# Kernel tuning notes

Hardware: AMD Instinct MI355X
Metric: run time of the kernel (lower is better)

Reference implementation:

```python
import jax, jax.numpy as jnp
import numpy as np

NB, H, C = 6, 4, 192
B, S, L = 2, 64, 256
VOCAB, ED = 24, 64


def setup_inputs() -> dict:
    key = jax.random.key(0)
    ks = iter(jax.random.split(key, 32))
    r = lambda sh: jax.random.normal(next(ks), sh, jnp.float32) * 0.02
    z = lambda sh: jnp.zeros(sh, jnp.float32)
    return {
        'tokens': jax.random.randint(next(ks), (B, S, L), 0, VOCAB, jnp.int32),
        'emb': r((VOCAB, ED)),
        'proj_w': r((C, ED)), 'proj_b': z((C,)),
        'ln_g': jnp.ones((NB, 3, C), jnp.float32), 'ln_b': z((NB, 3, C)),
        'wq': r((NB, 2, C, C)), 'wk': r((NB, 2, C, C)),
        'wv': r((NB, 2, C, C)), 'wo': r((NB, 2, C, C)),
        'bq': z((NB, 2, C)), 'bk': z((NB, 2, C)),
        'bv': z((NB, 2, C)), 'bo': z((NB, 2, C)),
        'ffn_w1': r((NB, 4 * C, C)), 'ffn_b1': z((NB, 4 * C)),
        'ffn_w2': r((NB, C, 4 * C)), 'ffn_b2': z((NB, C)),
        'pw_w': r((C,)), 'pw_b': z(()),
    }


def rotary(x):
    # ESM-style rotary embedding over positions along dim -2, feature dim last.
    d = x.shape[-1]
    inv = 1.0 / (10000.0 ** (jnp.arange(0, d, 2, dtype=jnp.float32) / d))
    t = jnp.arange(x.shape[-2], dtype=jnp.float32)
    f = t[:, None] * inv[None, :]                  # (pos, d/2)
    emb = jnp.concatenate([f, f], axis=-1)         # (pos, d)
    cos, sin = jnp.cos(emb), jnp.sin(emb)
    x1, x2 = jnp.split(x, 2, axis=-1)
    return x * cos + jnp.concatenate([-x2, x1], axis=-1) * sin


def ln_ch(x, g, b, eps=1e-5):
    # LayerNorm over channel axis 1 of (B,C,X,Y) (== transpose->LN->transpose).
    m = x.mean(axis=1, keepdims=True)
    v = jnp.var(x, axis=1, keepdims=True)
    return (x - m) * jax.lax.rsqrt(v + eps) * g[None, :, None, None] + b[None, :, None, None]


def lin_attn(x, wq, wk, wv, wo, bq, bk, bv, bo):
    # ScaledLinearAttention: elu+1 feature map, attends over dim -2 of (B,A,N,C).
    Bm, A, N, Cm = x.shape
    dh = Cm // H
    sh = lambda t: t.reshape(Bm, A, N, H, dh).transpose(0, 1, 3, 2, 4)  # (B,A,H,N,dh)
    q = sh(x @ wq.T + bq)
    k = sh(x @ wk.T + bk)
    v = sh(x @ wv.T + bv)
    q = (jax.nn.elu(q) + 1.0) / jnp.sqrt(jnp.float32(dh))
    k = jax.nn.elu(k) + 1.0
    kv = jnp.einsum('bahnd,bahne->bahde', k, v)
    z = 1.0 / (jnp.einsum('bahnd,bahd->bahn', q, k.sum(axis=-2)) + 1e-6)
    o = jnp.einsum('bahnd,bahde->bahne', q, kv) * z[..., None]
    o = o.transpose(0, 1, 3, 2, 4).reshape(Bm, A, N, Cm)
    return o @ wo.T + bo


def fwd(tokens, emb, proj_w, proj_b, ln_g, ln_b, wq, wk, wv, wo, bq, bk, bv, bo,
        ffn_w1, ffn_b1, ffn_w2, ffn_b2, pw_w, pw_b):
    x = emb[tokens]                    # (B,S,L,ED)
    x = x @ proj_w.T + proj_b          # (B,S,L,C)
    x = rotary(x)                      # rotary over L positions
    out = jnp.transpose(x, (0, 3, 1, 2))  # (B,C,S,L)
    for i in range(NB):
        # row attention (over L)
        h = ln_ch(out, ln_g[i, 0], ln_b[i, 0])
        h = jnp.transpose(h, (0, 2, 3, 1))  # (B,S,L,C)
        h = lin_attn(h, wq[i, 0], wk[i, 0], wv[i, 0], wo[i, 0],
                     bq[i, 0], bk[i, 0], bv[i, 0], bo[i, 0])
        out = out + jnp.transpose(h, (0, 3, 1, 2))
        # col attention (over S)
        h = ln_ch(out, ln_g[i, 1], ln_b[i, 1])
        h = jnp.transpose(h, (0, 3, 2, 1))  # (B,L,S,C)
        h = lin_attn(h, wq[i, 1], wk[i, 1], wv[i, 1], wo[i, 1],
                     bq[i, 1], bk[i, 1], bv[i, 1], bo[i, 1])
        out = out + jnp.transpose(h, (0, 3, 2, 1))
        # 1x1-conv FFN
        h = ln_ch(out, ln_g[i, 2], ln_b[i, 2])
        h = jnp.einsum('bcxy,oc->boxy', h, ffn_w1[i]) + ffn_b1[i][None, :, None, None]
        h = jax.nn.gelu(h, approximate=False)
        h = jnp.einsum('bcxy,oc->boxy', h, ffn_w2[i]) + ffn_b2[i][None, :, None, None]
        out = out + h
    o = jnp.einsum('bcxy,c->bxy', out, pw_w) + pw_b   # pwFNN 1x1 conv to 1 ch
    return jax.nn.sigmoid(jax.nn.softplus(o))


def reference(tokens, emb, proj_w, proj_b, ln_g, ln_b, wq, wk, wv, wo, bq, bk, bv, bo,
              ffn_w1, ffn_b1, ffn_w2, ffn_b2, pw_w, pw_b):
    return fwd(tokens, emb, proj_w, proj_b, ln_g, ln_b, wq, wk, wv, wo, bq, bk, bv, bo,
               ffn_w1, ffn_b1, ffn_w2, ffn_b2, pw_w, pw_b)
```

## Files before the change

kernel.cpp:

```cpp
#include <hip/hip_runtime.h>
#include <hip/hip_bf16.h>
#include <math.h>

#define NBLK 6
#define NH 4
#define CCH 192
#define BB 2
#define SS 64
#define LL 256
#define DH 48
#define NP (BB*SS*LL)
#define BUF ((size_t)NP*CCH)

typedef __attribute__((ext_vector_type(8))) short short8;
typedef __attribute__((ext_vector_type(4))) float float4v;
typedef __attribute__((ext_vector_type(2))) unsigned int uintx2;

__device__ __forceinline__ unsigned short f2b(float f) {
    union { float f; unsigned int u; } v; v.f = f;
    unsigned int r = v.u + 0x7FFF + ((v.u >> 16) & 1);
    return (unsigned short)(r >> 16);
}
__device__ __forceinline__ float b2f(unsigned short u) {
    union { unsigned int u; float f; } v; v.u = ((unsigned int)u) << 16;
    return v.f;
}
__device__ __forceinline__ unsigned int cvt_pk_bf16(float lo, float hi) {
    unsigned int r;
    asm("v_cvt_pk_bf16_f32 %0, %1, %2" : "=v"(r) : "v"(lo), "v"(hi));
    return r;
}
__device__ __forceinline__ void st2u(unsigned short* p0, unsigned short* p1, float a, float b) {
    unsigned int u = cvt_pk_bf16(a, b);
    *p0 = (unsigned short)u;
    *p1 = (unsigned short)(u >> 16);
}
__device__ __forceinline__ void xf_unpack(uintx2 u, float* f) {
    union { unsigned int x; float ff; } t;
    t.x = u[0] << 16;          f[0] = t.ff;
    t.x = u[0] & 0xffff0000u;  f[1] = t.ff;
    t.x = u[1] << 16;          f[2] = t.ff;
    t.x = u[1] & 0xffff0000u;  f[3] = t.ff;
}
__device__ __forceinline__ float gelu_f(float v) {
    float z = v * 0.7071067811865475f;
    float a = fabsf(z);
    float t = __builtin_amdgcn_rcpf(fmaf(0.3275911f, a, 1.0f));
    float p = fmaf(t, 1.061405429f, -1.453152027f);
    p = fmaf(t, p, 1.421413741f);
    p = fmaf(t, p, -0.284496736f);
    p = fmaf(t, p, 0.254829592f);
    p *= t;
    float e = __expf(-a * a);
    float er = fmaf(-p, e, 1.0f);
    er = __builtin_copysignf(er, z);
    return 0.5f * v * (1.0f + er);
}
__device__ __forceinline__ void async_lds16(const void* g, void* l) {
    __builtin_amdgcn_global_load_lds(
        (const __attribute__((address_space(1))) unsigned int*)g,
        (__attribute__((address_space(3))) unsigned int*)l, 16, 0, 0);
}

#define XF(p16, c) (((size_t)(p16) * 192 + (c)) << 4)

template<int N, int K>
__global__ void swz_conv(const float* __restrict__ src, unsigned short* __restrict__ dst, int layers) {
    int s = blockIdx.x * 256 + threadIdx.x;
    if (s >= layers * N * K) return;
    int li = s / (N * K);
    int t = s - li * (N * K);
    constexpr int KC = K / 32;
    int chunk = t >> 9, c = t & 511;
    int g = chunk / KC, sk = chunk - g * KC;
    int lane = c >> 3, ko = c & 7;
    int n = g * 16 + (lane & 15), k = sk * 32 + (lane >> 4) * 8 + ko;
    dst[s] = f2b(src[(size_t)li * N * K + (size_t)n * K + k]);
}
__global__ void wqkv_swz(const float* __restrict__ wq, const float* __restrict__ wk,
                         const float* __restrict__ wv, unsigned short* __restrict__ d) {
    int s = blockIdx.x * 256 + threadIdx.x;
    int wi = s / (576 * 192);
    int t = s - wi * 576 * 192;
    int chunk = t >> 9, c = t & 511;
    int g = chunk / 6, sk = chunk - g * 6;
    int lane = c >> 3, ko = c & 7;
    int n = g * 16 + (lane & 15), k = sk * 32 + (lane >> 4) * 8 + ko;
    int sg = n / 192, row = n - sg * 192;
    const float* src = (sg == 0) ? wq : (sg == 1) ? wk : wv;
    d[s] = f2b(src[(size_t)wi * 192 * 192 + (size_t)row * 192 + k]);
}
__global__ void bqkv_concat(const float* __restrict__ bq, const float* __restrict__ bk,
                            const float* __restrict__ bv, float* __restrict__ d) {
    int idx = blockIdx.x * 256 + threadIdx.x;
    if (idx >= NBLK * 2 * 576) return;
    int wi = idx / 576, n = idx - (idx / 576) * 576;
    int sg = n / 192, row = n - sg * 192;
    const float* src = (sg == 0) ? bq : (sg == 1) ? bk : bv;
    d[idx] = src[wi * CCH + row];
}

__global__ void gather_kernel(const int* __restrict__ tokens, const float* __restrict__ emb,
                              unsigned short* __restrict__ Eg) {
    int idx = blockIdx.x * 256 + threadIdx.x;
    int p = idx >> 6, c = idx & 63;
    Eg[idx] = f2b(emb[tokens[p] * 64 + c]);
}

__global__ __launch_bounds__(256) void rotary_ln_kernel(const float* __restrict__ Xt,
                                                        unsigned short* __restrict__ X,
                                                        unsigned short* __restrict__ Hn,
                                                        const float* __restrict__ g, const float* __restrict__ b) {
    int wave = threadIdx.x >> 6;
    int lane = threadIdx.x & 63;
    int p = blockIdx.x * 4 + wave;
    int l = p & (LL - 1);
    const float* xp = Xt + (size_t)p * CCH;
    float v[3];
    #pragma unroll
    for (int i = 0; i < 3; ++i) {
        int c = lane + i * 64;
        int j = c % 96;
        float inv = expf((float)(2 * j) * (-9.210340371976184f / 192.0f));
        float ang = (float)l * inv;
        float part = (c < 96) ? -xp[c + 96] : xp[c - 96];
        v[i] = xp[c] * cosf(ang) + part * sinf(ang);
    }
    float s = v[0] + v[1] + v[2];
    float qq = v[0] * v[0] + v[1] * v[1] + v[2] * v[2];
    #pragma unroll
    for (int off = 32; off; off >>= 1) {
        s += __shfl_xor(s, off, 64);
        qq += __shfl_xor(qq, off, 64);
    }
    float mean = s * (1.0f / 192.0f);
    float var = qq * (1.0f / 192.0f) - mean * mean;
    float r = rsqrtf(var + 1e-5f);
    unsigned short* hp = Hn + (size_t)p * CCH;
    const int p16 = p >> 4, pr = p & 15;
    #pragma unroll
    for (int i = 0; i < 3; ++i) {
        int c = lane + i * 64;
        X[XF(p16, c) + pr] = f2b(v[i]);
        hp[c] = f2b((v[i] - mean) * r * g[c] + b[c]);
    }
}

template<int MT, int EPI>
__global__ __launch_bounds__(256, (MT == 128) ? 3 : 4)
void mm192(const unsigned short* __restrict__ A, const unsigned short* __restrict__ Wsw,
           const float* __restrict__ bias,
           unsigned short* __restrict__ O0, unsigned short* __restrict__ O1,
           unsigned short* __restrict__ O2,
           float* __restrict__ Of,
           int M, int N, int K) {
    constexpr int NI = MT / 32;
    __shared__ __align__(16) unsigned char lds[(MT == 128) ? 51200 : 28672];
    const int tid = threadIdx.x;
    const int lane = tid & 63;
    const int w = tid >> 6;
    const int wm = w >> 1, wn = w & 1;
    const int m0 = blockIdx.y * MT;
    const int g0 = blockIdx.x * 12;
    const int q = lane >> 4;
    const int q8 = q << 3;
    const int r15 = lane & 15;
    const int KC = K >> 5;

    for (int c = w; c < (MT / 16) * KC; c += 4) {
        int g = c / KC, sk = c - g * KC;
        async_lds16(A + (size_t)(m0 + g * 16 + r15) * K + sk * 32 + q8, lds + c * 1024);
    }

    float4v acc[NI][6];
    #pragma unroll
    for (int i = 0; i < NI; ++i)
        #pragma unroll
        for (int j = 0; j < 6; ++j)
            acc[i][j] = (float4v){0.f, 0.f, 0.f, 0.f};

    __syncthreads();

    for (int sk = 0; sk < KC; ++sk) {
        short8 af[NI], wf[6];
        #pragma unroll
        for (int j = 0; j < 6; ++j)
            wf[j] = *(const short8*)(Wsw + (((size_t)(g0 + wn * 6 + j) * KC + sk) << 9) + lane * 8);
        #pragma unroll
        for (int i = 0; i < NI; ++i)
            af[i] = *(const short8*)(lds + (((wm * NI + i) * KC + sk) << 10) + lane * 16);
        #pragma unroll
        for (int i = 0; i < NI; ++i)
            #pragma unroll
            for (int j = 0; j < 6; ++j)
                acc[i][j] = __builtin_amdgcn_mfma_f32_16x16x32_bf16(af[i], wf[j], acc[i][j], 0, 0, 0);
    }

    const int nb = blockIdx.x * 192 + wn * 96 + r15;
    const int mb = m0 + wm * (MT / 2) + q * 4;

    if (EPI == 0) {
        const int bx = blockIdx.x;
        unsigned short* dst = (bx == 0) ? O0 : (bx == 1) ? O1 : O2;
        #pragma unroll
        for (int j = 0; j < 6; ++j) {
            int n = nb + j * 16;
            int col = wn * 96 + j * 16 + r15;
            float bv = bias[n];
            #pragma unroll
            for (int i = 0; i < NI; ++i) {
                int mrow = wm * (MT / 2) + i * 16 + q * 4;
                #pragma unroll
                for (int r = 0; r < 4; ++r) {
                    float v = acc[i][j][r] + bv;
                    if (bx < 2) v = (v > 0.f) ? v + 1.f : __expf(v);
                    if (bx == 0) v *= 0.14433756729740643f;
                    dst[(size_t)(m0 + mrow + r) * 192 + col] = f2b(v);
                }
            }
        }
    } else {
        #pragma unroll
        for (int j = 0; j < 6; ++j) {
            int n = nb + j * 16;
            float bv = bias[n];
            #pragma unroll
            for (int i = 0; i < NI; ++i) {
                int mrow = mb + i * 16;
                #pragma unroll
                for (int r = 0; r < 4; ++r)
                    Of[(size_t)(mrow + r) * N + n] = acc[i][j][r] + bv;
            }
        }
    }
}


__global__ __launch_bounds__(256, 2)
void wo_qkv(const unsigned short* __restrict__ Ho,
            const unsigned short* __restrict__ WOs, const float* __restrict__ BO,
            unsigned short* __restrict__ Xres,
            const float* __restrict__ lng, const float* __restrict__ lnb,
            const unsigned short* __restrict__ QKVs, const float* __restrict__ bqkv,
            unsigned short* __restrict__ Qb, unsigned short* __restrict__ Kb,
            unsigned short* __restrict__ Vb) {
    __shared__ __align__(16) unsigned char lds[51200];
    unsigned char* Lo = lds;
    float* lsum = (float*)(lds + 24576);
    float* lsq  = lsum + 256;
    unsigned char* Ap = lds + 26624;
    const int tid = threadIdx.x;
    const int lane = tid & 63;
    const int w = tid >> 6;
    const int m0 = blockIdx.x * 64;
    const int q = lane >> 4, q8 = q << 3, r15 = lane & 15;
    const int nb = w * 48 + r15;

    #pragma unroll
    for (int it = 0; it < 6; ++it) {
        int c = it * 4 + w;
        int g = c / 6, sk = c - g * 6;
        async_lds16(Ho + (size_t)(m0 + g * 16 + r15) * 192 + sk * 32 + q8, Lo + c * 1024);
    }
    __syncthreads();

    float4v acc[4][3];
    #pragma unroll
    for (int i = 0; i < 4; ++i)
        #pragma unroll
        for (int j = 0; j < 3; ++j)
            acc[i][j] = (float4v){0.f, 0.f, 0.f, 0.f};
    #pragma unroll
    for (int kk = 0; kk < 6; ++kk) {
        short8 af[4], wf[3];
        #pragma unroll
        for (int j = 0; j < 3; ++j)
            wf[j] = *(const short8*)(WOs + (((size_t)(w * 3 + j) * 6 + kk) << 9) + lane * 8);
        #pragma unroll
        for (int i = 0; i < 4; ++i)
            af[i] = *(const short8*)(Lo + ((i * 6 + kk) << 10) + lane * 16);
        #pragma unroll
        for (int i = 0; i < 4; ++i)
            #pragma unroll
            for (int j = 0; j < 3; ++j)
                acc[i][j] = __builtin_amdgcn_mfma_f32_16x16x32_bf16(af[i], wf[j], acc[i][j], 0, 0, 0);
    }

    #pragma unroll
    for (int j = 0; j < 3; ++j) {
        int n = nb + j * 16;
        float bv = BO[n];
        #pragma unroll
        for (int i = 0; i < 4; ++i) {
            unsigned short* xp = Xres + XF(blockIdx.x * 4 + i, n) + q * 4;
            uintx2 u = *(const uintx2*)xp;
            float f[4]; xf_unpack(u, f);
            #pragma unroll
            for (int r = 0; r < 4; ++r) acc[i][j][r] += bv + f[r];
            uintx2 o;
            o[0] = cvt_pk_bf16(acc[i][j][0], acc[i][j][1]);
            o[1] = cvt_pk_bf16(acc[i][j][2], acc[i][j][3]);
            *(uintx2*)xp = o;
        }
    }
    #pragma unroll
    for (int i = 0; i < 4; ++i)
        #pragma unroll
        for (int r = 0; r < 4; ++r) {
            float s1 = acc[i][0][r] + acc[i][1][r] + acc[i][2][r];
            float s2 = acc[i][0][r] * acc[i][0][r] + acc[i][1][r] * acc[i][1][r] + acc[i][2][r] * acc[i][2][r];
            #pragma unroll
            for (int off = 1; off < 16; off <<= 1) {
                s1 += __shfl_xor(s1, off, 64);
                s2 += __shfl_xor(s2, off, 64);
            }
            if (r15 == 0) {
                int rl = i * 16 + q * 4 + r;
                lsum[rl * 4 + w] = s1;
                lsq[rl * 4 + w] = s2;
            }
        }
    __syncthreads();
    #pragma unroll
    for (int i = 0; i < 4; ++i) {
        float mean[4], rstd[4];
        #pragma unroll
        for (int r = 0; r < 4; ++r) {
            int rl4 = (i * 16 + q * 4 + r) * 4;
            float s  = lsum[rl4] + lsum[rl4 + 1] + lsum[rl4 + 2] + lsum[rl4 + 3];
            float ss = lsq[rl4] + lsq[rl4 + 1] + lsq[rl4 + 2] + lsq[rl4 + 3];
            float m = s * (1.0f / 192.0f);
            mean[r] = m;
            rstd[r] = rsqrtf(ss * (1.0f / 192.0f) - m * m + 1e-5f);
        }
        #pragma unroll
        for (int j = 0; j < 3; ++j) {
            int h = nb + j * 16;
            float gg = lng[h], bb = lnb[h];
            unsigned short* ap = (unsigned short*)Ap + (i * 6 + (h >> 5)) * 512
                               + ((h >> 3) & 3) * 128 + (h & 7) + q * 32;
            float v0 = (acc[i][j][0] - mean[0]) * rstd[0] * gg + bb;
            float v1 = (acc[i][j][1] - mean[1]) * rstd[1] * gg + bb;
            float v2 = (acc[i][j][2] - mean[2]) * rstd[2] * gg + bb;
            float v3 = (acc[i][j][3] - mean[3]) * rstd[3] * gg + bb;
            st2u(ap, ap + 8, v0, v1);
            st2u(ap + 16, ap + 24, v2, v3);
        }
    }
    __syncthreads();

    for (int seg = 0; seg < 3; ++seg) {
        float4v a2[4][3];
        #pragma unroll
        for (int i = 0; i < 4; ++i)
            #pragma unroll
            for (int j = 0; j < 3; ++j)
                a2[i][j] = (float4v){0.f, 0.f, 0.f, 0.f};
        #pragma unroll
        for (int kk = 0; kk < 6; ++kk) {
            short8 af[4], wf[3];
            #pragma unroll
            for (int j = 0; j < 3; ++j)
                wf[j] = *(const short8*)(QKVs + (((size_t)(seg * 12 + w * 3 + j) * 6 + kk) << 9) + lane * 8);
            #pragma unroll
            for (int i = 0; i < 4; ++i)
                af[i] = *(const short8*)(Ap + ((i * 6 + kk) << 10) + lane * 16);
            #pragma unroll
            for (int i = 0; i < 4; ++i)
                #pragma unroll
                for (int j = 0; j < 3; ++j)
                    a2[i][j] = __builtin_amdgcn_mfma_f32_16x16x32_bf16(af[i], wf[j], a2[i][j], 0, 0, 0);
        }
        unsigned short* dst = (seg == 0) ? Qb : (seg == 1) ? Kb : Vb;
        #pragma unroll
        for (int j = 0; j < 3; ++j) {
            int n = nb + j * 16;
            float bv = bqkv[seg * 192 + n];
            #pragma unroll
            for (int i = 0; i < 4; ++i) {
                int mrow = m0 + i * 16 + q * 4;
                #pragma unroll
                for (int r = 0; r < 4; ++r) {
                    float x = a2[i][j][r] + bv;
                    if (seg < 2) x = (x > 0.f) ? x + 1.f : __expf(x);
                    if (seg == 0) x *= 0.14433756729740643f;
                    dst[(size_t)(mrow + r) * 192 + n] = f2b(x);
                }
            }
        }
    }
}

template<bool LASTB>
__global__ __launch_bounds__(256, 2)
void wo_ffn_qkv(const unsigned short* __restrict__ Ho,
                const unsigned short* __restrict__ WOs, const float* __restrict__ BO,
                unsigned short* __restrict__ Xres,
                const float* __restrict__ ln1g, const float* __restrict__ ln1b,
                const unsigned short* __restrict__ W1s, const float* __restrict__ B1,
                const unsigned short* __restrict__ W2s, const float* __restrict__ B2,
                const float* __restrict__ ln2g, const float* __restrict__ ln2b,
                const unsigned short* __restrict__ QKVs, const float* __restrict__ bqkv,
                unsigned short* __restrict__ Qb, unsigned short* __restrict__ Kb,
                unsigned short* __restrict__ Vb) {
    __shared__ __align__(16) unsigned char lds[51200];
    unsigned char* Lo = lds;
    float* lsum = (float*)(lds + 24576);
    float* lsq  = lsum + 256;
    unsigned char* Ap = lds + 26624;
    const int tid = threadIdx.x;
    const int lane = tid & 63;
    const int w = tid >> 6;
    const int m0 = blockIdx.x * 64;
    const int q = lane >> 4, q8 = q << 3, r15 = lane & 15;
    const int nb = w * 48 + r15;

    #pragma unroll
    for (int it = 0; it < 6; ++it) {
        int c = it * 4 + w;
        int g = c / 6, sk = c - g * 6;
        async_lds16(Ho + (size_t)(m0 + g * 16 + r15) * 192 + sk * 32 + q8, Lo + c * 1024);
    }
    __syncthreads();

    float4v xres[4][3];
    #pragma unroll
    for (int i = 0; i < 4; ++i)
        #pragma unroll
        for (int j = 0; j < 3; ++j)
            xres[i][j] = (float4v){0.f, 0.f, 0.f, 0.f};
    #pragma unroll
    for (int kk = 0; kk < 6; ++kk) {
        short8 af[4], wf[3];
        #pragma unroll
        for (int j = 0; j < 3; ++j)
            wf[j] = *(const short8*)(WOs + (((size_t)(w * 3 + j) * 6 + kk) << 9) + lane * 8);
        #pragma unroll
        for (int i = 0; i < 4; ++i)
            af[i] = *(const short8*)(Lo + ((i * 6 + kk) << 10) + lane * 16);
        #pragma unroll
        for (int i = 0; i < 4; ++i)
            #pragma unroll
            for (int j = 0; j < 3; ++j)
                xres[i][j] = __builtin_amdgcn_mfma_f32_16x16x32_bf16(af[i], wf[j], xres[i][j], 0, 0, 0);
    }
    #pragma unroll
    for (int j = 0; j < 3; ++j) {
        int n = nb + j * 16;
        float bv = BO[n];
        #pragma unroll
        for (int i = 0; i < 4; ++i) {
            const unsigned short* xp = Xres + XF(blockIdx.x * 4 + i, n) + q * 4;
            uintx2 u = *(const uintx2*)xp;
            float f[4]; xf_unpack(u, f);
            #pragma unroll
            for (int r = 0; r < 4; ++r) xres[i][j][r] += bv + f[r];
        }
    }
    #pragma unroll
    for (int i = 0; i < 4; ++i)
        #pragma unroll
        for (int r = 0; r < 4; ++r) {
            float s1 = xres[i][0][r] + xres[i][1][r] + xres[i][2][r];
            float s2 = xres[i][0][r] * xres[i][0][r] + xres[i][1][r] * xres[i][1][r] + xres[i][2][r] * xres[i][2][r];
            #pragma unroll
            for (int off = 1; off < 16; off <<= 1) {
                s1 += __shfl_xor(s1, off, 64);
                s2 += __shfl_xor(s2, off, 64);
            }
            if (r15 == 0) {
                int rl = i * 16 + q * 4 + r;
                lsum[rl * 4 + w] = s1;
                lsq[rl * 4 + w] = s2;
            }
        }
    __syncthreads();
    #pragma unroll
    for (int i = 0; i < 4; ++i) {
        float mean[4], rstd[4];
        #pragma unroll
        for (int r = 0; r < 4; ++r) {
            int rl4 = (i * 16 + q * 4 + r) * 4;
            float s  = lsum[rl4] + lsum[rl4 + 1] + lsum[rl4 + 2] + lsum[rl4 + 3];
            float ss = lsq[rl4] + lsq[rl4 + 1] + lsq[rl4 + 2] + lsq[rl4 + 3];
            float m = s * (1.0f / 192.0f);
            mean[r] = m;
            rstd[r] = rsqrtf(ss * (1.0f / 192.0f) - m * m + 1e-5f);
        }
        #pragma unroll
        for (int j = 0; j < 3; ++j) {
            int h = nb + j * 16;
            float gg = ln1g[h], bb = ln1b[h];
            unsigned short* ap = (unsigned short*)Ap + (i * 6 + (h >> 5)) * 512
                               + ((h >> 3) & 3) * 128 + (h & 7) + q * 32;
            float v0 = (xres[i][j][0] - mean[0]) * rstd[0] * gg + bb;
            float v1 = (xres[i][j][1] - mean[1]) * rstd[1] * gg + bb;
            float v2 = (xres[i][j][2] - mean[2]) * rstd[2] * gg + bb;
            float v3 = (xres[i][j][3] - mean[3]) * rstd[3] * gg + bb;
            st2u(ap, ap + 8, v0, v1);
            st2u(ap + 16, ap + 24, v2, v3);
        }
    }
    __syncthreads();

    float4v acc2[4][3];
    #pragma unroll
    for (int i = 0; i < 4; ++i)
        #pragma unroll
        for (int j = 0; j < 3; ++j)
            acc2[i][j] = (float4v){0.f, 0.f, 0.f, 0.f};
    for (int hc = 0; hc < 4; ++hc) {
        float4v acc1[4][3];
        #pragma unroll
        for (int i = 0; i < 4; ++i)
            #pragma unroll
            for (int j = 0; j < 3; ++j)
                acc1[i][j] = (float4v){0.f, 0.f, 0.f, 0.f};
        #pragma unroll
        for (int kk = 0; kk < 6; ++kk) {
            short8 af[4], wf[3];
            #pragma unroll
            for (int j = 0; j < 3; ++j)
                wf[j] = *(const short8*)(W1s + (((size_t)(hc * 12 + w * 3 + j) * 6 + kk) << 9) + lane * 8);
            #pragma unroll
            for (int i = 0; i < 4; ++i)
                af[i] = *(const short8*)(Ap + ((i * 6 + kk) << 10) + lane * 16);
            #pragma unroll
            for (int i = 0; i < 4; ++i)
                #pragma unroll
                for (int j = 0; j < 3; ++j)
                    acc1[i][j] = __builtin_amdgcn_mfma_f32_16x16x32_bf16(af[i], wf[j], acc1[i][j], 0, 0, 0);
        }
        __syncthreads();
        #pragma unroll
        for (int i = 0; i < 4; ++i)
            #pragma unroll
            for (int j = 0; j < 3; ++j) {
                int h = nb + j * 16;
                float bv = B1[hc * 192 + h];
                unsigned short* lp = (unsigned short*)Lo + (i * 6 + (h >> 5)) * 512
                                   + ((h >> 3) & 3) * 128 + (h & 7) + q * 32;
                float v0 = gelu_f(acc1[i][j][0] + bv);
                float v1 = gelu_f(acc1[i][j][1] + bv);
                float v2 = gelu_f(acc1[i][j][2] + bv);
                float v3 = gelu_f(acc1[i][j][3] + bv);
                st2u(lp, lp + 8, v0, v1);
                st2u(lp + 16, lp + 24, v2, v3);
            }
        __syncthreads();
        #pragma unroll
        for (int kk = 0; kk < 6; ++kk) {
            short8 af[4], wf[3];
            #pragma unroll
            for (int j = 0; j < 3; ++j)
                wf[j] = *(const short8*)(W2s + (((size_t)(w * 3 + j) * 24 + hc * 6 + kk) << 9) + lane * 8);
            #pragma unroll
            for (int i = 0; i < 4; ++i)
                af[i] = *(const short8*)(Lo + ((i * 6 + kk) << 10) + lane * 16);
            #pragma unroll
            for (int i = 0; i < 4; ++i)
                #pragma unroll
                for (int j = 0; j < 3; ++j)
                    acc2[i][j] = __builtin_amdgcn_mfma_f32_16x16x32_bf16(af[i], wf[j], acc2[i][j], 0, 0, 0);
        }
    }

    #pragma unroll
    for (int j = 0; j < 3; ++j) {
        int n = nb + j * 16;
        float bv = B2[n];
        #pragma unroll
        for (int i = 0; i < 4; ++i) {
            #pragma unroll
            for (int r = 0; r < 4; ++r)
                xres[i][j][r] += acc2[i][j][r] + bv;
            unsigned short* xp = Xres + XF(blockIdx.x * 4 + i, n) + q * 4;
            uintx2 o;
            o[0] = cvt_pk_bf16(xres[i][j][0], xres[i][j][1]);
            o[1] = cvt_pk_bf16(xres[i][j][2], xres[i][j][3]);
            *(uintx2*)xp = o;
        }
    }
    if (LASTB) return;

    #pragma unroll
    for (int i = 0; i < 4; ++i)
        #pragma unroll
        for (int r = 0; r < 4; ++r) {
            float s1 = xres[i][0][r] + xres[i][1][r] + xres[i][2][r];
            float s2 = xres[i][0][r] * xres[i][0][r] + xres[i][1][r] * xres[i][1][r] + xres[i][2][r] * xres[i][2][r];
            #pragma unroll
            for (int off = 1; off < 16; off <<= 1) {
                s1 += __shfl_xor(s1, off, 64);
                s2 += __shfl_xor(s2, off, 64);
            }
            if (r15 == 0) {
                int rl = i * 16 + q * 4 + r;
                lsum[rl * 4 + w] = s1;
                lsq[rl * 4 + w] = s2;
            }
        }
    __syncthreads();
    #pragma unroll
    for (int i = 0; i < 4; ++i) {
        float mean[4], rstd[4];
        #pragma unroll
        for (int r = 0; r < 4; ++r) {
            int rl4 = (i * 16 + q * 4 + r) * 4;
            float s  = lsum[rl4] + lsum[rl4 + 1] + lsum[rl4 + 2] + lsum[rl4 + 3];
            float ss = lsq[rl4] + lsq[rl4 + 1] + lsq[rl4 + 2] + lsq[rl4 + 3];
            float m = s * (1.0f / 192.0f);
            mean[r] = m;
            rstd[r] = rsqrtf(ss * (1.0f / 192.0f) - m * m + 1e-5f);
        }
        #pragma unroll
        for (int j = 0; j < 3; ++j) {
            int h = nb + j * 16;
            float gg = ln2g[h], bb = ln2b[h];
            unsigned short* ap = (unsigned short*)Ap + (i * 6 + (h >> 5)) * 512
                               + ((h >> 3) & 3) * 128 + (h & 7) + q * 32;
            float v0 = (xres[i][j][0] - mean[0]) * rstd[0] * gg + bb;
            float v1 = (xres[i][j][1] - mean[1]) * rstd[1] * gg + bb;
            float v2 = (xres[i][j][2] - mean[2]) * rstd[2] * gg + bb;
            float v3 = (xres[i][j][3] - mean[3]) * rstd[3] * gg + bb;
            st2u(ap, ap + 8, v0, v1);
            st2u(ap + 16, ap + 24, v2, v3);
        }
    }
    __syncthreads();

    for (int seg = 0; seg < 3; ++seg) {
        float4v a2[4][3];
        #pragma unroll
        for (int i = 0; i < 4; ++i)
            #pragma unroll
            for (int j = 0; j < 3; ++j)
                a2[i][j] = (float4v){0.f, 0.f, 0.f, 0.f};
        #pragma unroll
        for (int kk = 0; kk < 6; ++kk) {
            short8 af[4], wf[3];
            #pragma unroll
            for (int j = 0; j < 3; ++j)
                wf[j] = *(const short8*)(QKVs + (((size_t)(seg * 12 + w * 3 + j) * 6 + kk) << 9) + lane * 8);
            #pragma unroll
            for (int i = 0; i < 4; ++i)
                af[i] = *(const short8*)(Ap + ((i * 6 + kk) << 10) + lane * 16);
            #pragma unroll
            for (int i = 0; i < 4; ++i)
                #pragma unroll
                for (int j = 0; j < 3; ++j)
                    a2[i][j] = __builtin_amdgcn_mfma_f32_16x16x32_bf16(af[i], wf[j], a2[i][j], 0, 0, 0);
        }
        unsigned short* dst = (seg == 0) ? Qb : (seg == 1) ? Kb : Vb;
        #pragma unroll
        for (int j = 0; j < 3; ++j) {
            int n = nb + j * 16;
            float bv = bqkv[seg * 192 + n];
            #pragma unroll
            for (int i = 0; i < 4; ++i) {
                int mrow = m0 + i * 16 + q * 4;
                #pragma unroll
                for (int r = 0; r < 4; ++r) {
                    float x = a2[i][j][r] + bv;
                    if (seg < 2) x = (x > 0.f) ? x + 1.f : __expf(x);
                    if (seg == 0) x *= 0.14433756729740643f;
                    dst[(size_t)(mrow + r) * 192 + n] = f2b(x);
                }
            }
        }
    }
}

template<int N, int MSTR>
__global__ __launch_bounds__(256) void attn_axial(const unsigned short* __restrict__ Qb,
                                                  const unsigned short* __restrict__ Kb,
                                                  const unsigned short* __restrict__ Vb,
                                                  unsigned short* __restrict__ O) {
    __shared__ unsigned short KV[32][400];
    __shared__ unsigned short kvs[4][64][72];
    unsigned char* kvb = (unsigned char*)KV;
    const int tid = threadIdx.x;
    const int lane = tid & 63;
    const int w = tid >> 6;
    const int q = lane >> 4, r15 = lane & 15, q8 = q * 8;
    size_t base;
    if (MSTR == 1) base = (size_t)blockIdx.x * N;
    else           base = (size_t)(blockIdx.x >> 8) * 16384 + (blockIdx.x & 255);

    unsigned int* kz = (unsigned int*)&kvs[w][0][0];
    #pragma unroll
    for (int ii = 0; ii < 36; ++ii) kz[lane + ii * 64] = 0;

    short8 onesf;
    #pragma unroll
    for (int e = 0; e < 8; ++e) onesf[e] = (short)0x3F80;

    float4v kv[3][4];
    #pragma unroll
    for (int i = 0; i < 3; ++i)
        #pragma unroll
        for (int j = 0; j < 4; ++j)
            kv[i][j] = (float4v){0.f, 0.f, 0.f, 0.f};

    for (int ks = 0; ks < N; ks += 32) {
        #pragma unroll
        for (int it = 0; it < 6; ++it) {
            int cc = tid + it * 256;
            int row = cc / 48, c8 = cc - (cc / 48) * 48;
            size_t poff = (base + (size_t)(ks + row) * MSTR) * 192;
            const unsigned short* gp = (c8 < 24) ? (Kb + poff + c8 * 8) : (Vb + poff + (c8 - 24) * 8);
            int ba = (row * 800 + c8 * 16) ^ (((row >> 3) & 3) << 5);
            *(short8*)(kvb + ba) = *(const short8*)gp;
        }
        __syncthreads();
        short8 af[3], bf[3];
        #pragma unroll
        for (int t = 0; t < 3; ++t) {
            #pragma unroll
            for (int j = 0; j < 8; ++j) {
                int row = q8 + j;
                int sw = ((row >> 3) & 3) << 5;
                af[t][j] = *(short*)(kvb + ((row * 800 + (w * 48 + t * 16 + r15) * 2) ^ sw));
                bf[t][j] = *(short*)(kvb + ((row * 800 + 384 + (w * 48 + t * 16 + r15) * 2) ^ sw));
            }
        }
        #pragma unroll
        for (int i = 0; i < 3; ++i) {
            #pragma unroll
            for (int j = 0; j < 3; ++j)
                kv[i][j] = __builtin_amdgcn_mfma_f32_16x16x32_bf16(af[i], bf[j], kv[i][j], 0, 0, 0);
            kv[i][3] = __builtin_amdgcn_mfma_f32_16x16x32_bf16(af[i], onesf, kv[i][3], 0, 0, 0);
        }
        __syncthreads();
    }

    #pragma unroll
    for (int i = 0; i < 3; ++i) {
        #pragma unroll
        for (int j = 0; j < 3; ++j)
            #pragma unroll
            for (int r = 0; r < 4; ++r)
                kvs[w][j * 16 + r15][i * 16 + q * 4 + r] = f2b(kv[i][j][r]);
        if (r15 == 0)
            #pragma unroll
            for (int r = 0; r < 4; ++r)
                kvs[w][48][i * 16 + q * 4 + r] = f2b(kv[i][3][r]);
    }

    short8 bkv[2][4];
    #pragma unroll
    for (int kk = 0; kk < 2; ++kk)
        #pragma unroll
        for (int t = 0; t < 4; ++t)
            bkv[kk][t] = *(const short8*)&kvs[w][t * 16 + r15][kk * 32 + q8];

    for (int mt = 0; mt < N / 16; ++mt) {
        float4v o[4];
        #pragma unroll
        for (int t = 0; t < 4; ++t) o[t] = (float4v){0.f, 0.f, 0.f, 0.f};
        #pragma unroll
        for (int kk = 0; kk < 2; ++kk) {
            const unsigned short* qp = Qb + (base + (size_t)(mt * 16 + r15) * MSTR) * 192
                                       + w * 48 + kk * 32 + q8;
            short8 aq = *(const short8*)qp;
            #pragma unroll
            for (int t = 0; t < 4; ++t)
                o[t] = __builtin_amdgcn_mfma_f32_16x16x32_bf16(aq, bkv[kk][t], o[t], 0, 0, 0);
        }
        #pragma unroll
        for (int r = 0; r < 4; ++r) {
            float den = __shfl(o[3][r], q << 4);
            float z = 1.0f / (den + 1e-6f);
            int n = mt * 16 + q * 4 + r;
            unsigned short* op = O + (base + (size_t)n * MSTR) * 192 + w * 48;
            #pragma unroll
            for (int t = 0; t < 3; ++t)
                op[t * 16 + r15] = f2b(o[t][r] * z);
        }
    }
}

__global__ __launch_bounds__(256) void final_kernel(const unsigned short* __restrict__ X,
                                                    const float* __restrict__ pw_w,
                                                    const float* __restrict__ pw_b, float* __restrict__ out) {
    int wave = threadIdx.x >> 6;
    int lane = threadIdx.x & 63;
    int p = blockIdx.x * 4 + wave;
    const unsigned short* xp = X + XF(p >> 4, 0) + (p & 15);
    float s = b2f(xp[(size_t)lane << 4]) * pw_w[lane]
            + b2f(xp[(size_t)(lane + 64) << 4]) * pw_w[lane + 64]
            + b2f(xp[(size_t)(lane + 128) << 4]) * pw_w[lane + 128];
    #pragma unroll
    for (int off = 32; off; off >>= 1) s += __shfl_xor(s, off, 64);
    if (lane == 0) {
        float o = s + pw_b[0];
        float e = expf(o);
        out[p] = 1.0f - 1.0f / (2.0f + e);
    }
}

extern "C" void kernel_launch(void* const* d_in, const int* in_sizes, int n_in,
                              void* d_out, int out_size, void* d_ws, size_t ws_size,
                              hipStream_t stream) {
    const int*   tokens = (const int*)  d_in[0];
    const float* emb    = (const float*)d_in[1];
    const float* proj_w = (const float*)d_in[2];
    const float* proj_b = (const float*)d_in[3];
    const float* ln_g   = (const float*)d_in[4];
    const float* ln_b   = (const float*)d_in[5];
    const float* wq     = (const float*)d_in[6];
    const float* wk     = (const float*)d_in[7];
    const float* wv     = (const float*)d_in[8];
    const float* wo     = (const float*)d_in[9];
    const float* bq     = (const float*)d_in[10];
    const float* bk     = (const float*)d_in[11];
    const float* bv     = (const float*)d_in[12];
    const float* bo     = (const float*)d_in[13];
    const float* ffn_w1 = (const float*)d_in[14];
    const float* ffn_b1 = (const float*)d_in[15];
    const float* ffn_w2 = (const float*)d_in[16];
    const float* ffn_b2 = (const float*)d_in[17];
    const float* pw_w   = (const float*)d_in[18];
    const float* pw_b   = (const float*)d_in[19];

    unsigned short* X    = (unsigned short*)d_ws;
    unsigned short* Ho   = X + BUF;
    unsigned short* Qb   = Ho + BUF;
    unsigned short* Kb   = Qb + BUF;
    unsigned short* Vb   = Kb + BUF;
    unsigned short* Eg   = Vb + BUF;
    unsigned short* wqkvb = Eg + (size_t)NP * 64;
    const int QKVSZ = NBLK * 2 * 576 * CCH;
    const int WSZ   = NBLK * 2 * CCH * CCH;
    const int FSZ   = NBLK * 768 * CCH;
    unsigned short* wob = wqkvb + QKVSZ;
    unsigned short* w1b = wob + WSZ;
    unsigned short* w2b = w1b + FSZ;
    unsigned short* pjb = w2b + FSZ;
    float* bqkvb = (float*)(pjb + 12288 + 32);
    float* Xt = (float*)Qb;

    wqkv_swz<<<QKVSZ / 256, 256, 0, stream>>>(wq, wk, wv, wqkvb);
    bqkv_concat<<<27, 256, 0, stream>>>(bq, bk, bv, bqkvb);
    swz_conv<192, 192><<<(WSZ + 255) / 256, 256, 0, stream>>>(wo, wob, NBLK * 2);
    swz_conv<768, 192><<<(FSZ + 255) / 256, 256, 0, stream>>>(ffn_w1, w1b, NBLK);
    swz_conv<192, 768><<<(FSZ + 255) / 256, 256, 0, stream>>>(ffn_w2, w2b, NBLK);
    swz_conv<192, 64><<<48, 256, 0, stream>>>(proj_w, pjb, 1);

    gather_kernel<<<NP * 64 / 256, 256, 0, stream>>>(tokens, emb, Eg);
    mm192<64, 1><<<dim3(1, NP / 64), 256, 0, stream>>>(Eg, pjb, proj_b,
                                                       nullptr, nullptr, nullptr, Xt, NP, CCH, 64);
    rotary_ln_kernel<<<NP / 4, 256, 0, stream>>>(Xt, X, Ho, ln_g, ln_b);
    mm192<128, 0><<<dim3(3, NP / 128), 256, 0, stream>>>(Ho, wqkvb, bqkvb,
                                                         Qb, Kb, Vb, nullptr, NP, 576, CCH);

    for (int i = 0; i < NBLK; ++i) {
        size_t wi0 = (size_t)(i * 2), wi1 = wi0 + 1;
        attn_axial<LL, 1><<<BB * SS, 256, 0, stream>>>(Qb, Kb, Vb, Ho);
        wo_qkv<<<NP / 64, 256, 0, stream>>>(Ho, wob + wi0 * CCH * CCH, bo + wi0 * CCH, X,
                                            ln_g + (size_t)(i * 3 + 1) * CCH, ln_b + (size_t)(i * 3 + 1) * CCH,
                                            wqkvb + wi1 * 576 * CCH, bqkvb + wi1 * 576, Qb, Kb, Vb);
        attn_axial<SS, LL><<<BB * LL, 256, 0, stream>>>(Qb, Kb, Vb, Ho);
        if (i < NBLK - 1) {
            size_t wn0 = (size_t)((i + 1) * 2);
            wo_ffn_qkv<false><<<NP / 64, 256, 0, stream>>>(
                Ho, wob + wi1 * CCH * CCH, bo + wi1 * CCH, X,
                ln_g + (size_t)(i * 3 + 2) * CCH, ln_b + (size_t)(i * 3 + 2) * CCH,
                w1b + (size_t)i * 768 * CCH, ffn_b1 + (size_t)i * 768,
                w2b + (size_t)i * CCH * 768, ffn_b2 + (size_t)i * CCH,
                ln_g + (size_t)((i + 1) * 3) * CCH, ln_b + (size_t)((i + 1) * 3) * CCH,
                wqkvb + wn0 * 576 * CCH, bqkvb + wn0 * 576, Qb, Kb, Vb);
        } else {
            wo_ffn_qkv<true><<<NP / 64, 256, 0, stream>>>(
                Ho, wob + wi1 * CCH * CCH, bo + wi1 * CCH, X,
                ln_g + (size_t)(i * 3 + 2) * CCH, ln_b + (size_t)(i * 3 + 2) * CCH,
                w1b + (size_t)i * 768 * CCH, ffn_b1 + (size_t)i * 768,
                w2b + (size_t)i * CCH * 768, ffn_b2 + (size_t)i * CCH,
                nullptr, nullptr, nullptr, nullptr, nullptr, nullptr, nullptr);
        }
    }
    final_kernel<<<NP / 4, 256, 0, stream>>>(X, pw_w, pw_b, (float*)d_out);
}
```

Measured before the change: 885.8 us.

## Split row attention across 8 waves and halve wo_qkv row tile

Adds an attn_row8 kernel for the row axis. It uses 512 threads per block: two groups of four waves each accumulate K^T V and the K-sum over half of the 256 positions, then combine the partials through LDS before computing outputs. The wo_qkv kernel now processes 32 rows per block instead of 64, with half the LDS and launch bounds raised to 4 blocks per SM, to increase occupancy and block count. The cost is more weight fragment reloads per row in wo_qkv, and a larger LDS footprint plus an extra reduction step in the new attention kernel.

```diff
diff --git a/kernel.cpp b/kernel.cpp
--- a/kernel.cpp
+++ b/kernel.cpp
@@ -236,7 +236,7 @@
 }
 
 
-__global__ __launch_bounds__(256, 2)
+__global__ __launch_bounds__(256, 4)
 void wo_qkv(const unsigned short* __restrict__ Ho,
             const unsigned short* __restrict__ WOs, const float* __restrict__ BO,
             unsigned short* __restrict__ Xres,
@@ -244,43 +244,43 @@
             const unsigned short* __restrict__ QKVs, const float* __restrict__ bqkv,
             unsigned short* __restrict__ Qb, unsigned short* __restrict__ Kb,
             unsigned short* __restrict__ Vb) {
-    __shared__ __align__(16) unsigned char lds[51200];
+    __shared__ __align__(16) unsigned char lds[25600];
     unsigned char* Lo = lds;
-    float* lsum = (float*)(lds + 24576);
-    float* lsq  = lsum + 256;
-    unsigned char* Ap = lds + 26624;
+    float* lsum = (float*)(lds + 12288);
+    float* lsq  = lsum + 128;
+    unsigned char* Ap = lds + 13312;
     const int tid = threadIdx.x;
     const int lane = tid & 63;
     const int w = tid >> 6;
-    const int m0 = blockIdx.x * 64;
+    const int m0 = blockIdx.x * 32;
     const int q = lane >> 4, q8 = q << 3, r15 = lane & 15;
     const int nb = w * 48 + r15;
 
     #pragma unroll
-    for (int it = 0; it < 6; ++it) {
+    for (int it = 0; it < 3; ++it) {
         int c = it * 4 + w;
         int g = c / 6, sk = c - g * 6;
         async_lds16(Ho + (size_t)(m0 + g * 16 + r15) * 192 + sk * 32 + q8, Lo + c * 1024);
     }
     __syncthreads();
 
-    float4v acc[4][3];
-    #pragma unroll
-    for (int i = 0; i < 4; ++i)
+    float4v acc[2][3];
+    #pragma unroll
+    for (int i = 0; i < 2; ++i)
         #pragma unroll
         for (int j = 0; j < 3; ++j)
             acc[i][j] = (float4v){0.f, 0.f, 0.f, 0.f};
     #pragma unroll
     for (int kk = 0; kk < 6; ++kk) {
-        short8 af[4], wf[3];
+        short8 af[2], wf[3];
         #pragma unroll
         for (int j = 0; j < 3; ++j)
             wf[j] = *(const short8*)(WOs + (((size_t)(w * 3 + j) * 6 + kk) << 9) + lane * 8);
         #pragma unroll
-        for (int i = 0; i < 4; ++i)
+        for (int i = 0; i < 2; ++i)
             af[i] = *(const short8*)(Lo + ((i * 6 + kk) << 10) + lane * 16);
         #pragma unroll
-        for (int i = 0; i < 4; ++i)
+        for (int i = 0; i < 2; ++i)
             #pragma unroll
             for (int j = 0; j < 3; ++j)
                 acc[i][j] = __builtin_amdgcn_mfma_f32_16x16x32_bf16(af[i], wf[j], acc[i][j], 0, 0, 0);
@@ -291,8 +291,8 @@
         int n = nb + j * 16;
         float bv = BO[n];
         #pragma unroll
-        for (int i = 0; i < 4; ++i) {
-            unsigned short* xp = Xres + XF(blockIdx.x * 4 + i, n) + q * 4;
+        for (int i = 0; i < 2; ++i) {
+            unsigned short* xp = Xres + XF(blockIdx.x * 2 + i, n) + q * 4;
             uintx2 u = *(const uintx2*)xp;
             float f[4]; xf_unpack(u, f);
             #pragma unroll
@@ -304,7 +304,7 @@
         }
     }
     #pragma unroll
-    for (int i = 0; i < 4; ++i)
+    for (int i = 0; i < 2; ++i)
         #pragma unroll
         for (int r = 0; r < 4; ++r) {
             float s1 = acc[i][0][r] + acc[i][1][r] + acc[i][2][r];
@@ -322,7 +322,7 @@
         }
     __syncthreads();
     #pragma unroll
-    for (int i = 0; i < 4; ++i) {
+    for (int i = 0; i < 2; ++i) {
         float mean[4], rstd[4];
         #pragma unroll
         for (int r = 0; r < 4; ++r) {
@@ -350,23 +350,23 @@
     __syncthreads();
 
     for (int seg = 0; seg < 3; ++seg) {
-        float4v a2[4][3];
-        #pragma unroll
-        for (int i = 0; i < 4; ++i)
+        float4v a2[2][3];
+        #pragma unroll
+        for (int i = 0; i < 2; ++i)
             #pragma unroll
             for (int j = 0; j < 3; ++j)
                 a2[i][j] = (float4v){0.f, 0.f, 0.f, 0.f};
         #pragma unroll
         for (int kk = 0; kk < 6; ++kk) {
-            short8 af[4], wf[3];
+            short8 af[2], wf[3];
             #pragma unroll
             for (int j = 0; j < 3; ++j)
                 wf[j] = *(const short8*)(QKVs + (((size_t)(seg * 12 + w * 3 + j) * 6 + kk) << 9) + lane * 8);
             #pragma unroll
-            for (int i = 0; i < 4; ++i)
+            for (int i = 0; i < 2; ++i)
                 af[i] = *(const short8*)(Ap + ((i * 6 + kk) << 10) + lane * 16);
             #pragma unroll
-            for (int i = 0; i < 4; ++i)
+            for (int i = 0; i < 2; ++i)
                 #pragma unroll
                 for (int j = 0; j < 3; ++j)
                     a2[i][j] = __builtin_amdgcn_mfma_f32_16x16x32_bf16(af[i], wf[j], a2[i][j], 0, 0, 0);
@@ -377,7 +377,7 @@
             int n = nb + j * 16;
             float bv = bqkv[seg * 192 + n];
             #pragma unroll
-            for (int i = 0; i < 4; ++i) {
+            for (int i = 0; i < 2; ++i) {
                 int mrow = m0 + i * 16 + q * 4;
                 #pragma unroll
                 for (int r = 0; r < 4; ++r) {
@@ -671,6 +671,138 @@
     }
 }
 
+__global__ __launch_bounds__(512) void attn_row8(const unsigned short* __restrict__ Qb,
+                                                 const unsigned short* __restrict__ Kb,
+                                                 const unsigned short* __restrict__ Vb,
+                                                 unsigned short* __restrict__ O) {
+    __shared__ __align__(16) unsigned char lds[100352];
+    unsigned char* kvb = lds;
+    float* kvsum = (float*)(lds + 51200);
+    unsigned short* kvs = (unsigned short*)lds;
+    const int tid = threadIdx.x;
+    const int lane = tid & 63;
+    const int w = tid >> 6;
+    const int h = w & 3;
+    const int half = w >> 2;
+    const int q = lane >> 4, r15 = lane & 15, q8 = q * 8;
+    const size_t base = (size_t)blockIdx.x * 256;
+
+    short8 onesf;
+    #pragma unroll
+    for (int e = 0; e < 8; ++e) onesf[e] = (short)0x3F80;
+
+    float4v kv[3][4];
+    #pragma unroll
+    for (int i = 0; i < 3; ++i)
+        #pragma unroll
+        for (int j = 0; j < 4; ++j)
+            kv[i][j] = (float4v){0.f, 0.f, 0.f, 0.f};
+
+    for (int ks = 0; ks < 128; ks += 32) {
+        #pragma unroll
+        for (int it = 0; it < 6; ++it) {
+            int cc = it * 512 + tid;
+            int gr = cc / 48, c8 = cc - gr * 48;
+            int hf = gr >> 5, row = gr & 31;
+            size_t poff = (base + (size_t)(ks + hf * 128 + row)) * 192;
+            const unsigned short* gp = (c8 < 24) ? (Kb + poff + c8 * 8) : (Vb + poff + (c8 - 24) * 8);
+            int ba = hf * 25600 + ((row * 800 + c8 * 16) ^ (((row >> 3) & 3) << 5));
+            *(short8*)(kvb + ba) = *(const short8*)gp;
+        }
+        __syncthreads();
+        short8 af[3], bf[3];
+        const unsigned char* hb = kvb + half * 25600;
+        #pragma unroll
+        for (int t = 0; t < 3; ++t) {
+            #pragma unroll
+            for (int j = 0; j < 8; ++j) {
+                int row = q8 + j;
+                int sw = ((row >> 3) & 3) << 5;
+                af[t][j] = *(const short*)(hb + ((row * 800 + (h * 48 + t * 16 + r15) * 2) ^ sw));
+                bf[t][j] = *(const short*)(hb + ((row * 800 + 384 + (h * 48 + t * 16 + r15) * 2) ^ sw));
+            }
+        }
+        #pragma unroll
+        for (int i = 0; i < 3; ++i) {
+            #pragma unroll
+            for (int j = 0; j < 3; ++j)
+                kv[i][j] = __builtin_amdgcn_mfma_f32_16x16x32_bf16(af[i], bf[j], kv[i][j], 0, 0, 0);
+            kv[i][3] = __builtin_amdgcn_mfma_f32_16x16x32_bf16(af[i], onesf, kv[i][3], 0, 0, 0);
+        }
+        __syncthreads();
+    }
+
+    if (half) {
+        float* kp = kvsum + h * 3072;
+        #pragma unroll
+        for (int i = 0; i < 3; ++i)
+            #pragma unroll
+            for (int j = 0; j < 4; ++j)
+                #pragma unroll
+                for (int r = 0; r < 4; ++r)
+                    kp[((i * 4 + j) * 4 + r) * 64 + lane] = kv[i][j][r];
+    }
+    __syncthreads();
+    if (!half) {
+        const float* kp = kvsum + h * 3072;
+        #pragma unroll
+        for (int i = 0; i < 3; ++i)
+            #pragma unroll
+            for (int j = 0; j < 4; ++j)
+                #pragma unroll
+                for (int r = 0; r < 4; ++r)
+                    kv[i][j][r] += kp[((i * 4 + j) * 4 + r) * 64 + lane];
+        unsigned int* kz = (unsigned int*)(kvs + h * 4608);
+        #pragma unroll
+        for (int ii = 0; ii < 36; ++ii) kz[lane + ii * 64] = 0;
+        #pragma unroll
+        for (int i = 0; i < 3; ++i) {
+            #pragma unroll
+            for (int j = 0; j < 3; ++j)
+                #pragma unroll
+                for (int r = 0; r < 4; ++r)
+                    kvs[(h * 64 + j * 16 + r15) * 72 + i * 16 + q * 4 + r] = f2b(kv[i][j][r]);
+            if (r15 == 0)
+                #pragma unroll
+                for (int r = 0; r < 4; ++r)
+                    kvs[(h * 64 + 48) * 72 + i * 16 + q * 4 + r] = f2b(kv[i][3][r]);
+        }
+    }
+    __syncthreads();
+
+    short8 bkv[2][4];
+    #pragma unroll
+    for (int kk = 0; kk < 2; ++kk)
+        #pragma unroll
+        for (int t = 0; t < 4; ++t)
+            bkv[kk][t] = *(const short8*)&kvs[(h * 64 + t * 16 + r15) * 72 + kk * 32 + q8];
+
+    for (int mt = half * 8; mt < half * 8 + 8; ++mt) {
+        float4v o[4];
+        #pragma unroll
+        for (int t = 0; t < 4; ++t) o[t] = (float4v){0.f, 0.f, 0.f, 0.f};
+        #pragma unroll
+        for (int kk = 0; kk < 2; ++kk) {
+            const unsigned short* qp = Qb + (base + (size_t)(mt * 16 + r15)) * 192
+                                       + h * 48 + kk * 32 + q8;
+            short8 aq = *(const short8*)qp;
+            #pragma unroll
+            for (int t = 0; t < 4; ++t)
+                o[t] = __builtin_amdgcn_mfma_f32_16x16x32_bf16(aq, bkv[kk][t], o[t], 0, 0, 0);
+        }
+        #pragma unroll
+        for (int r = 0; r < 4; ++r) {
+            float den = __shfl(o[3][r], q << 4);
+            float z = 1.0f / (den + 1e-6f);
+            int n = mt * 16 + q * 4 + r;
+            unsigned short* op = O + (base + (size_t)n) * 192 + h * 48;
+            #pragma unroll
+            for (int t = 0; t < 3; ++t)
+                op[t * 16 + r15] = f2b(o[t][r] * z);
+        }
+    }
+}
+
 template<int N, int MSTR>
 __global__ __launch_bounds__(256) void attn_axial(const unsigned short* __restrict__ Qb,
                                                   const unsigned short* __restrict__ Kb,
@@ -856,8 +988,8 @@
 
     for (int i = 0; i < NBLK; ++i) {
         size_t wi0 = (size_t)(i * 2), wi1 = wi0 + 1;
-        attn_axial<LL, 1><<<BB * SS, 256, 0, stream>>>(Qb, Kb, Vb, Ho);
-        wo_qkv<<<NP / 64, 256, 0, stream>>>(Ho, wob + wi0 * CCH * CCH, bo + wi0 * CCH, X,
+        attn_row8<<<BB * SS, 512, 0, stream>>>(Qb, Kb, Vb, Ho);
+        wo_qkv<<<NP / 32, 256, 0, stream>>>(Ho, wob + wi0 * CCH * CCH, bo + wi0 * CCH, X,
                                             ln_g + (size_t)(i * 3 + 1) * CCH, ln_b + (size_t)(i * 3 + 1) * CCH,
                                             wqkvb + wi1 * 576 * CCH, bqkvb + wi1 * 576, Qb, Kb, Vb);
         attn_axial<SS, LL><<<BB * LL, 256, 0, stream>>>(Qb, Kb, Vb, Ho);
```

After: 875.4 us. About the same (-1.2%).
